# Kernel optimization log

Measured on AMD Instinct MI355X. Metric: run time of the kernel, lower is better.

Reference implementation:

```python
import jax, jax.numpy as jnp
import numpy as np
import math

B, WIN, C_IN, C_OUT = 8, 512, 38, 38
D_MODEL, N_HEADS, E_LAYERS, D_FF = 512, 8, 3, 512
EH = D_MODEL // N_HEADS
LN_EPS = 1e-3  # keras LayerNormalization default


def setup_inputs() -> dict:
    key = jax.random.key(0)
    ks = jax.random.split(key, 24)
    s = 0.02
    rn = lambda k, sh: jax.random.normal(k, sh, jnp.float32) * s
    L, d, H = E_LAYERS, D_MODEL, N_HEADS
    return {
        "x": jax.random.normal(ks[0], (B, WIN, C_IN), jnp.float32),
        "conv_k": rn(ks[1], (3, C_IN, d)),
        "Wq": rn(ks[2], (L, d, d)), "bq": jnp.zeros((L, d), jnp.float32),
        "Wk": rn(ks[3], (L, d, d)), "bk": jnp.zeros((L, d), jnp.float32),
        "Wv": rn(ks[4], (L, d, d)), "bv": jnp.zeros((L, d), jnp.float32),
        "Ws": rn(ks[5], (L, d, H)), "bs": jnp.zeros((L, H), jnp.float32),
        "Wo": rn(ks[6], (L, d, d)), "bo": jnp.zeros((L, d), jnp.float32),
        "W1": rn(ks[7], (L, d, D_FF)), "b1": jnp.zeros((L, D_FF), jnp.float32),
        "W2": rn(ks[8], (L, D_FF, d)), "b2": jnp.zeros((L, d), jnp.float32),
        "ln1_g": jnp.ones((L, d), jnp.float32), "ln1_b": jnp.zeros((L, d), jnp.float32),
        "ln2_g": jnp.ones((L, d), jnp.float32), "ln2_b": jnp.zeros((L, d), jnp.float32),
        "lnf_g": jnp.ones((d,), jnp.float32), "lnf_b": jnp.zeros((d,), jnp.float32),
        "Wp": rn(ks[9], (d, C_OUT)), "bp": jnp.zeros((C_OUT,), jnp.float32),
    }


def _layernorm(x, g, b):
    mu = jnp.mean(x, axis=-1, keepdims=True)
    var = jnp.mean((x - mu) ** 2, axis=-1, keepdims=True)
    return (x - mu) * jax.lax.rsqrt(var + LN_EPS) * g + b


def _pos_embedding():
    pos = jnp.arange(WIN, dtype=jnp.float32)[:, None]
    div = jnp.exp(jnp.arange(0, D_MODEL, 2, dtype=jnp.float32) * (-math.log(10000.0) / D_MODEL))
    # interleave sin at even idx, cos at odd idx
    return jnp.stack([jnp.sin(pos * div), jnp.cos(pos * div)], axis=-1).reshape(WIN, D_MODEL)


def reference(x, conv_k, Wq, bq, Wk, bk, Wv, bv, Ws, bs, Wo, bo,
              W1, b1, W2, b2, ln1_g, ln1_b, ln2_g, ln2_b, lnf_g, lnf_b, Wp, bp):
    # --- DataEmbedding: wrap-pad then Conv1D(k=3, valid), plus sinusoidal PE ---
    xp = jnp.concatenate([x[:, -1:], x, x[:, :1]], axis=1)
    h = jax.lax.conv_general_dilated(xp, conv_k, window_strides=(1,), padding='VALID',
                                     dimension_numbers=('NWC', 'WIO', 'NWC'))
    h = h + _pos_embedding()[None]

    idx = jnp.arange(WIN, dtype=jnp.float32)
    dist = jnp.abs(idx[:, None] - idx[None, :])
    scale = 1.0 / math.sqrt(EH)
    inv_sqrt_2pi = 1.0 / math.sqrt(2.0 * math.pi)

    series_l, prior_l, sigma_l = [], [], []
    for i in range(E_LAYERS):
        q = (h @ Wq[i] + bq[i]).reshape(B, WIN, N_HEADS, EH)
        k = (h @ Wk[i] + bk[i]).reshape(B, WIN, N_HEADS, EH)
        v = (h @ Wv[i] + bv[i]).reshape(B, WIN, N_HEADS, EH)
        sig = h @ Ws[i] + bs[i]

        scores = jnp.einsum('blhe,bshe->bhls', q, k)  # mask_flag=False in model
        series = jax.nn.softmax(scores * scale, axis=-1)  # [B, H, L, S]

        sg = jnp.transpose(sig, (0, 2, 1))               # [B, H, L]
        sg = jax.nn.sigmoid(sg * 5.0) + 1e-5
        sg = jnp.power(3.0, sg) - 1.0
        sg4 = jnp.broadcast_to(sg[..., None], (B, N_HEADS, WIN, WIN))
        prior = inv_sqrt_2pi / sg4 * jnp.exp(-(dist ** 2) / (2.0 * sg4 ** 2))

        attn_out = jnp.einsum('bhls,bshd->blhd', series, v).reshape(B, WIN, D_MODEL)
        h = _layernorm(h + attn_out @ Wo[i] + bo[i], ln1_g[i], ln1_b[i])
        y = jax.nn.gelu(h @ W1[i] + b1[i], approximate=False)
        y = y @ W2[i] + b2[i]
        h = _layernorm(h + y, ln2_g[i], ln2_b[i])

        series_l.append(series); prior_l.append(prior); sigma_l.append(sg4)

    h = _layernorm(h, lnf_g, lnf_b)
    out = h @ Wp + bp
    return (out, jnp.stack(series_l), jnp.stack(prior_l), jnp.stack(sigma_l))
```

## Files before the change

### kernel.cpp

```cpp
#include <hip/hip_runtime.h>
#include <math.h>


typedef unsigned short ushort;
typedef __attribute__((ext_vector_type(8))) ushort ushort8;
typedef __attribute__((ext_vector_type(4))) ushort ushort4v;
typedef __attribute__((ext_vector_type(8))) short short8;
typedef __attribute__((ext_vector_type(4))) float float4v;

__device__ inline ushort f2bf(float f) {
  union { float f; unsigned u; } v; v.f = f;
  return (ushort)((v.u + 0x7fffu + ((v.u >> 16) & 1u)) >> 16);
}

__device__ inline void gload16(const void* g, void* l) {
  __builtin_amdgcn_global_load_lds(
      (const __attribute__((address_space(1))) unsigned int*)g,
      (__attribute__((address_space(3))) unsigned int*)l, 16, 0, 0);
}

__global__ __launch_bounds__(512) void embed_kernel(const float* __restrict__ x,
                                                    const float* __restrict__ ck,
                                                    float* __restrict__ h,
                                                    ushort* __restrict__ hb) {
  int bt = blockIdx.x;
  int b = bt >> 9, t = bt & 511;
  int co = threadIdx.x;
  __shared__ float xs[3][38];
  if (co < 114) {
    int w = co / 38, ci = co - w * 38;
    int r = (t - 1 + w + 512) & 511;
    xs[w][ci] = x[((long)(b << 9) + r) * 38 + ci];
  }
  __syncthreads();
  float acc = 0.f;
#pragma unroll
  for (int w = 0; w < 3; ++w)
#pragma unroll
    for (int ci = 0; ci < 38; ++ci)
      acc = fmaf(xs[w][ci], ck[(w * 38 + ci) * 512 + co], acc);
  float div = expf((float)(co & ~1) * (-9.210340371976184f / 512.f));
  float ang = (float)t * div;
  float pe = (co & 1) ? cosf(ang) : sinf(ang);
  float o = acc + pe;
  h[(long)bt * 512 + co] = o;
  hb[(long)bt * 512 + co] = f2bf(o);
}

__global__ __launch_bounds__(256) void wcvt_kernel(const float* __restrict__ W,
                                                   ushort* __restrict__ Wt,
                                                   long lstride) {
  int l = blockIdx.z;
  int n = blockIdx.x * 256 + threadIdx.x;
  int k0 = blockIdx.y * 8;
  const float* w = W + (long)l * 262144;
  ushort* o = Wt + (long)l * lstride;
  ushort8 v;
#pragma unroll
  for (int i = 0; i < 8; ++i) v[i] = f2bf(w[(long)(k0 + i) * 512 + n]);
  *(ushort8*)&o[(long)n * 512 + k0] = v;
}

__global__ __launch_bounds__(512) void bcat_kernel(const float* __restrict__ bq,
                                                   const float* __restrict__ bk,
                                                   const float* __restrict__ bv,
                                                   float* __restrict__ bqkv) {
  int l = blockIdx.x, t = threadIdx.x;
  bqkv[l * 1536 + t] = bq[l * 512 + t];
  bqkv[l * 1536 + 512 + t] = bk[l * 512 + t];
  bqkv[l * 1536 + 1024 + t] = bv[l * 512 + t];
}

__global__ __launch_bounds__(512) void wst_kernel(const float* __restrict__ Ws,
                                                  float* __restrict__ WsT) {
  int l = blockIdx.x, k = threadIdx.x;
#pragma unroll
  for (int hh = 0; hh < 8; ++hh)
    WsT[(long)l * 4096 + hh * 512 + k] = Ws[(long)l * 4096 + k * 8 + hh];
}

template <bool GELU_, bool CBF16, bool VST>
__global__ __launch_bounds__(256) void gemm_bt(
    const ushort* __restrict__ A, int lda,
    const ushort* __restrict__ B, int ldb,
    const float* __restrict__ bias,
    void* __restrict__ Cv, int ldc, int K,
    ushort* __restrict__ vTout) {
  __shared__ ushort As[2][4096];
  __shared__ ushort Bs[2][2048];
  int t = threadIdx.x;
  int m0 = blockIdx.y * 128, n0 = blockIdx.x * 64;
  int w = t >> 6, lane = t & 63;
  int wr = (w >> 1) * 64, wc = (w & 1) * 32;
  int fm = lane & 15, q4 = lane >> 4;
  float4v acc[4][2];
#pragma unroll
  for (int i = 0; i < 4; ++i)
#pragma unroll
    for (int j = 0; j < 2; ++j) acc[i][j] = (float4v){0.f, 0.f, 0.f, 0.f};

  int kk = (lane & 3) * 8;
  const ushort* ga0 = &A[(long)(m0 + w * 32 + (lane >> 2)) * lda + kk];
  const ushort* ga1 = ga0 + (long)16 * lda;
  const ushort* gb = &B[(long)(n0 + w * 16 + (lane >> 2)) * ldb + kk];

  auto stage = [&](int bi) {
    gload16(ga0, &As[bi][w * 1024]);
    gload16(ga1, &As[bi][w * 1024 + 512]);
    gload16(gb, &Bs[bi][w * 512]);
    ga0 += 32; ga1 += 32; gb += 32;
  };
  auto compute = [&](int bi) {
    short8 a[4], bfr[2];
#pragma unroll
    for (int i = 0; i < 4; ++i)
      a[i] = *(const short8*)&As[bi][(wr + 16 * i + fm) * 32 + q4 * 8];
#pragma unroll
    for (int j = 0; j < 2; ++j)
      bfr[j] = *(const short8*)&Bs[bi][(wc + 16 * j + fm) * 32 + q4 * 8];
#pragma unroll
    for (int i = 0; i < 4; ++i)
#pragma unroll
      for (int j = 0; j < 2; ++j)
        acc[i][j] = __builtin_amdgcn_mfma_f32_16x16x32_bf16(a[i], bfr[j], acc[i][j], 0, 0, 0);
  };

  stage(0);
  __syncthreads();
#pragma unroll 1
  for (int k0 = 0; k0 < K; k0 += 64) {
    stage(1);
    compute(0);
    __syncthreads();
    if (k0 + 64 < K) stage(0);
    compute(1);
    __syncthreads();
  }

#pragma unroll
  for (int j = 0; j < 2; ++j) {
    int col = n0 + wc + 16 * j + fm;
    float bv = bias ? bias[col] : 0.f;
#pragma unroll
    for (int i = 0; i < 4; ++i) {
      int row0 = m0 + wr + 16 * i + q4 * 4;
      float vv[4];
#pragma unroll
      for (int r = 0; r < 4; ++r) {
        float v = acc[i][j][r] + bv;
        if (GELU_) v = 0.5f * v * (1.f + erff(v * 0.7071067811865476f));
        vv[r] = v;
        if (CBF16)
          ((ushort*)Cv)[(long)(row0 + r) * ldc + col] = f2bf(v);
        else
          ((float*)Cv)[(long)(row0 + r) * ldc + col] = v;
      }
      if (VST && n0 >= 1024) {
        int d = (col - 1024) & 63;
        int hh = (n0 - 1024) >> 6;
        int bb = row0 >> 9, s0 = row0 & 511;
        ushort4v pk;
#pragma unroll
        for (int r = 0; r < 4; ++r) pk[r] = f2bf(vv[r]);
        *(ushort4v*)&vTout[((long)(bb * 8 + hh) * 64 + d) * 512 + s0] = pk;
      }
    }
  }
}

__global__ __launch_bounds__(256, 2) void attn_fused(
    const ushort* __restrict__ qkv, const ushort* __restrict__ vT,
    const float* __restrict__ h, const float* __restrict__ WsT,
    const float* __restrict__ bsw,
    float* __restrict__ series, float* __restrict__ prior,
    float* __restrict__ sigma, ushort* __restrict__ t1b) {
  __shared__ ushort Ps[32 * 520];
  __shared__ float red[128];
  __shared__ float sgc[96];

  int t = threadIdx.x;
  int m0 = blockIdx.x * 32;
  int bh = blockIdx.y;
  int b = bh >> 3, hh = bh & 7;
  int w = t >> 6, lane = t & 63;
  int fm = lane & 15, q4 = lane >> 4;
  int wc = w * 128;
  long rowg = (long)b * 512;

  {
    int r = t >> 3, p = t & 7;
    const float* hrow = &h[(rowg + m0 + r) * 512 + p * 64];
    const float* wcol = &WsT[hh * 512 + p * 64];
    float s = 0.f;
#pragma unroll
    for (int i = 0; i < 16; ++i) {
      float4 hv = *(const float4*)&hrow[i * 4];
      float4 wv = *(const float4*)&wcol[i * 4];
      s += hv.x * wv.x + hv.y * wv.y + hv.z * wv.z + hv.w * wv.w;
    }
    s += __shfl_xor(s, 1); s += __shfl_xor(s, 2); s += __shfl_xor(s, 4);
    if (p == 0) {
      float xv = s + bsw[hh];
      float sig = 1.f / (1.f + __expf(-5.f * xv)) + 1e-5f;
      float sgv = expm1f(sig * 1.0986122886681098f);
      sgc[r * 3] = sgv;
      sgc[r * 3 + 1] = 0.3989422804014327f / sgv;
      sgc[r * 3 + 2] = 1.f / sgv;
    }
  }

  float4v acc[2][8];
#pragma unroll
  for (int i = 0; i < 2; ++i)
#pragma unroll
    for (int j = 0; j < 8; ++j) acc[i][j] = (float4v){0.f, 0.f, 0.f, 0.f};

  const ushort* qbase = &qkv[(rowg + m0) * 1536 + hh * 64];
  const ushort* kbase = &qkv[rowg * 1536 + 512 + hh * 64];
#pragma unroll
  for (int ks = 0; ks < 2; ++ks) {
    int ko = ks * 32 + q4 * 8;
    short8 a[2], bfr[8];
#pragma unroll
    for (int i = 0; i < 2; ++i)
      a[i] = *(const short8*)&qbase[(long)(16 * i + fm) * 1536 + ko];
#pragma unroll
    for (int j = 0; j < 8; ++j)
      bfr[j] = *(const short8*)&kbase[(long)(wc + 16 * j + fm) * 1536 + ko];
#pragma unroll
    for (int i = 0; i < 2; ++i)
#pragma unroll
      for (int j = 0; j < 8; ++j)
        acc[i][j] = __builtin_amdgcn_mfma_f32_16x16x32_bf16(a[i], bfr[j], acc[i][j], 0, 0, 0);
  }

#pragma unroll
  for (int i = 0; i < 2; ++i)
#pragma unroll
    for (int j = 0; j < 8; ++j)
#pragma unroll
      for (int r = 0; r < 4; ++r) acc[i][j][r] *= 0.125f;

  float mrow[2][4];
#pragma unroll
  for (int i = 0; i < 2; ++i)
#pragma unroll
    for (int r = 0; r < 4; ++r) {
      float m = acc[i][0][r];
#pragma unroll
      for (int j = 1; j < 8; ++j) m = fmaxf(m, acc[i][j][r]);
#pragma unroll
      for (int off = 1; off < 16; off <<= 1) m = fmaxf(m, __shfl_xor(m, off));
      mrow[i][r] = m;
    }
  if (fm == 0) {
#pragma unroll
    for (int i = 0; i < 2; ++i)
#pragma unroll
      for (int r = 0; r < 4; ++r)
        red[(16 * i + q4 * 4 + r) * 4 + w] = mrow[i][r];
  }
  __syncthreads();
#pragma unroll
  for (int i = 0; i < 2; ++i)
#pragma unroll
    for (int r = 0; r < 4; ++r) {
      const float* rp = &red[(16 * i + q4 * 4 + r) * 4];
      mrow[i][r] = fmaxf(fmaxf(rp[0], rp[1]), fmaxf(rp[2], rp[3]));
    }
  float lrow[2][4];
#pragma unroll
  for (int i = 0; i < 2; ++i)
#pragma unroll
    for (int r = 0; r < 4; ++r) {
      float s = 0.f;
#pragma unroll
      for (int j = 0; j < 8; ++j) {
        float e = __expf(acc[i][j][r] - mrow[i][r]);
        acc[i][j][r] = e;
        s += e;
      }
#pragma unroll
      for (int off = 1; off < 16; off <<= 1) s += __shfl_xor(s, off);
      lrow[i][r] = s;
    }
  __syncthreads();
  if (fm == 0) {
#pragma unroll
    for (int i = 0; i < 2; ++i)
#pragma unroll
      for (int r = 0; r < 4; ++r)
        red[(16 * i + q4 * 4 + r) * 4 + w] = lrow[i][r];
  }
  __syncthreads();
#pragma unroll
  for (int i = 0; i < 2; ++i)
#pragma unroll
    for (int r = 0; r < 4; ++r) {
      const float* rp = &red[(16 * i + q4 * 4 + r) * 4];
      lrow[i][r] = 1.f / (rp[0] + rp[1] + rp[2] + rp[3]);
    }

  float* serp = series + ((long)bh << 18);
#pragma unroll
  for (int i = 0; i < 2; ++i)
#pragma unroll
    for (int r = 0; r < 4; ++r) {
      int row = 16 * i + q4 * 4 + r;
      float inv = lrow[i][r];
#pragma unroll
      for (int j = 0; j < 8; ++j) {
        int col = wc + 16 * j + fm;
        float v = acc[i][j][r] * inv;
        serp[(long)(m0 + row) * 512 + col] = v;
        Ps[row * 520 + col] = f2bf(v);
      }
    }
  __syncthreads();

  float4v acc2[2] = {{0.f, 0.f, 0.f, 0.f}, {0.f, 0.f, 0.f, 0.f}};
  int wn = w * 16;
  const ushort* vbase = &vT[((long)bh * 64 + wn + fm) * 512];
#pragma unroll
  for (int c = 0; c < 8; ++c) {
#pragma unroll
    for (int ks = 0; ks < 2; ++ks) {
      int ko = ks * 32 + q4 * 8;
      short8 b2 = *(const short8*)&vbase[c * 64 + ko];
#pragma unroll
      for (int i = 0; i < 2; ++i) {
        short8 a2 = *(const short8*)&Ps[(16 * i + fm) * 520 + c * 64 + ko];
        acc2[i] = __builtin_amdgcn_mfma_f32_16x16x32_bf16(a2, b2, acc2[i], 0, 0, 0);
      }
    }
  }
#pragma unroll
  for (int i = 0; i < 2; ++i)
#pragma unroll
    for (int r = 0; r < 4; ++r)
      t1b[(rowg + m0 + 16 * i + q4 * 4 + r) * 512 + hh * 64 + wn + fm] =
          f2bf(acc2[i][r]);

  float* prip = prior + ((long)bh << 18);
  float* sigp = sigma + ((long)bh << 18);
  for (int it = t; it < 4096; it += 256) {
    int row = it >> 7;
    int c4 = (it & 127) << 2;
    float sgv = sgc[row * 3], inv = sgc[row * 3 + 1], rinv = sgc[row * 3 + 2];
    float ig = (float)(m0 + row);
    float4 pv, sv;
#pragma unroll
    for (int e = 0; e < 4; ++e) {
      float dd = ig - (float)(c4 + e);
      float rr = dd * rinv;
      ((float*)&pv)[e] = inv * __expf(-0.5f * rr * rr);
      ((float*)&sv)[e] = sgv;
    }
    *(float4*)&prip[(long)(m0 + row) * 512 + c4] = pv;
    *(float4*)&sigp[(long)(m0 + row) * 512 + c4] = sv;
  }
}

__global__ __launch_bounds__(256) void ln_kernel(const float* __restrict__ x,
                                                 const float* __restrict__ delta,
                                                 const float* __restrict__ g,
                                                 const float* __restrict__ bb,
                                                 float* __restrict__ out,
                                                 ushort* __restrict__ hb) {
  long row = blockIdx.x;
  int tid = threadIdx.x;
  int c = tid * 2;
  float2 xv = *(const float2*)&x[row * 512 + c];
  if (delta) {
    float2 dv = *(const float2*)&delta[row * 512 + c];
    xv.x += dv.x; xv.y += dv.y;
  }
  float s = xv.x + xv.y;
  float q = xv.x * xv.x + xv.y * xv.y;
#pragma unroll
  for (int off = 1; off < 64; off <<= 1) {
    s += __shfl_xor(s, off);
    q += __shfl_xor(q, off);
  }
  __shared__ float red[8];
  int wid = tid >> 6;
  if ((tid & 63) == 0) { red[wid] = s; red[wid + 4] = q; }
  __syncthreads();
  float S = red[0] + red[1] + red[2] + red[3];
  float Q = red[4] + red[5] + red[6] + red[7];
  float mean = S * (1.f / 512.f);
  float var = Q * (1.f / 512.f) - mean * mean;
  float rstd = rsqrtf(var + 1e-3f);
  float2 o;
  o.x = (xv.x - mean) * rstd * g[c] + bb[c];
  o.y = (xv.y - mean) * rstd * g[c + 1] + bb[c + 1];
  *(float2*)&out[row * 512 + c] = o;
  if (hb) {
    unsigned pk = ((unsigned)f2bf(o.y) << 16) | (unsigned)f2bf(o.x);
    ((unsigned*)hb)[row * 256 + tid] = pk;
  }
}

template <int NOUT>
__global__ __launch_bounds__(256) void gemm_smallN(const float* __restrict__ A,
                                                   const float* __restrict__ W,
                                                   const float* __restrict__ bias,
                                                   float* __restrict__ C) {
  long row = (long)blockIdx.x * 4 + (threadIdx.x >> 6);
  int lane = threadIdx.x & 63;
  float acc[NOUT];
#pragma unroll
  for (int j = 0; j < NOUT; ++j) acc[j] = 0.f;
  for (int k = lane; k < 512; k += 64) {
    float a = A[row * 512 + k];
    const float* wr = W + (long)k * NOUT;
#pragma unroll
    for (int j = 0; j < NOUT; ++j) acc[j] = fmaf(a, wr[j], acc[j]);
  }
#pragma unroll
  for (int j = 0; j < NOUT; ++j)
#pragma unroll
    for (int off = 32; off; off >>= 1) acc[j] += __shfl_xor(acc[j], off);
  if (lane == 0) {
#pragma unroll
    for (int j = 0; j < NOUT; ++j) C[row * NOUT + j] = acc[j] + bias[j];
  }
}

extern "C" void kernel_launch(void* const* d_in, const int* in_sizes, int n_in,
                              void* d_out, int out_size, void* d_ws, size_t ws_size,
                              hipStream_t stream) {
  (void)in_sizes; (void)n_in; (void)out_size; (void)ws_size;
  const float* x    = (const float*)d_in[0];
  const float* ck   = (const float*)d_in[1];
  const float* Wq   = (const float*)d_in[2];
  const float* bq   = (const float*)d_in[3];
  const float* Wk   = (const float*)d_in[4];
  const float* bk   = (const float*)d_in[5];
  const float* Wv   = (const float*)d_in[6];
  const float* bv   = (const float*)d_in[7];
  const float* Wsw  = (const float*)d_in[8];
  const float* bsw  = (const float*)d_in[9];
  const float* Wo   = (const float*)d_in[10];
  const float* bo   = (const float*)d_in[11];
  const float* W1   = (const float*)d_in[12];
  const float* b1   = (const float*)d_in[13];
  const float* W2   = (const float*)d_in[14];
  const float* b2   = (const float*)d_in[15];
  const float* ln1g = (const float*)d_in[16];
  const float* ln1b = (const float*)d_in[17];
  const float* ln2g = (const float*)d_in[18];
  const float* ln2b = (const float*)d_in[19];
  const float* lnfg = (const float*)d_in[20];
  const float* lnfb = (const float*)d_in[21];
  const float* Wp   = (const float*)d_in[22];
  const float* bp   = (const float*)d_in[23];
  float* out = (float*)d_out;

  float* h    = (float*)d_ws;
  float* t1   = h + 2097152;
  float* t2   = t1 + 2097152;
  float* wst  = t2 + 2097152;
  float* bqkv = wst + 32768;
  ushort* qkv  = (ushort*)(bqkv + 4608);
  ushort* wqkv = qkv + 6291456;
  ushort* wo3  = wqkv + 2359296;
  ushort* w13  = wo3 + 786432;
  ushort* w23  = w13 + 786432;
  ushort* t1b = (ushort*)t1;
  ushort* hb  = (ushort*)(t1 + 1048576);
  ushort* vT  = (ushort*)t2;

  float* series0 = out + 155648;
  float* prior0  = out + 50487296;
  float* sigma0  = out + 100818944;

  dim3 gW(2, 64, 3);
  wcvt_kernel<<<gW, 256, 0, stream>>>(Wq, wqkv, 786432);
  wcvt_kernel<<<gW, 256, 0, stream>>>(Wk, wqkv + 262144, 786432);
  wcvt_kernel<<<gW, 256, 0, stream>>>(Wv, wqkv + 524288, 786432);
  wcvt_kernel<<<gW, 256, 0, stream>>>(Wo, wo3, 262144);
  wcvt_kernel<<<gW, 256, 0, stream>>>(W1, w13, 262144);
  wcvt_kernel<<<gW, 256, 0, stream>>>(W2, w23, 262144);
  bcat_kernel<<<3, 512, 0, stream>>>(bq, bk, bv, bqkv);
  wst_kernel<<<3, 512, 0, stream>>>(Wsw, wst);

  embed_kernel<<<4096, 512, 0, stream>>>(x, ck, h, hb);

  dim3 gQKV(24, 32, 1);
  dim3 gFull(8, 32, 1);
  dim3 gAttn(16, 64, 1);

  for (int l = 0; l < 3; ++l) {
    float* ser = series0 + (long)l * 16777216;
    float* pri = prior0  + (long)l * 16777216;
    float* sgm = sigma0  + (long)l * 16777216;

    gemm_bt<false, true, true><<<gQKV, 256, 0, stream>>>(
        hb, 512, wqkv + (long)l * 786432, 512, bqkv + l * 1536, qkv, 1536, 512, vT);
    attn_fused<<<gAttn, 256, 0, stream>>>(qkv, vT, h, wst + (long)l * 4096,
                                          bsw + (long)l * 8, ser, pri, sgm, t1b);
    gemm_bt<false, false, false><<<gFull, 256, 0, stream>>>(
        t1b, 512, wo3 + (long)l * 262144, 512, bo + (long)l * 512, t2, 512, 512, nullptr);
    ln_kernel<<<4096, 256, 0, stream>>>(h, t2, ln1g + l * 512, ln1b + l * 512, h, hb);
    gemm_bt<true, true, false><<<gFull, 256, 0, stream>>>(
        hb, 512, w13 + (long)l * 262144, 512, b1 + (long)l * 512, t1b, 512, 512, nullptr);
    gemm_bt<false, false, false><<<gFull, 256, 0, stream>>>(
        t1b, 512, w23 + (long)l * 262144, 512, b2 + (long)l * 512, t2, 512, 512, nullptr);
    ln_kernel<<<4096, 256, 0, stream>>>(h, t2, ln2g + l * 512, ln2b + l * 512, h, hb);
  }

  ln_kernel<<<4096, 256, 0, stream>>>(h, nullptr, lnfg, lnfb, t1, nullptr);
  gemm_smallN<38><<<1024, 256, 0, stream>>>(t1, Wp, bp, out);
}
```

Before: 1.037 ms.

## Rewrite GEMM to hold full B tile in LDS, fuse prep and final LN-projection

Replaces the double-buffered bf16 GEMM with a kernel that loads the entire 64x512 weight tile into swizzled LDS once and streams A from global memory into 32x32x16 MFMAs with two split-K accumulators. Weight conversion, bias concatenation and Ws transposes are merged into two launches, and the weight layout is XOR-swizzled to avoid LDS bank conflicts. The final LayerNorm is fused into the output projection kernel. This aims to cut launch overhead and per-k-step syncs, at the cost of 64KB LDS per block limiting occupancy and unstaged A loads from global memory.

Result: slower. 1.063 ms (+2.5%).

```diff
diff --git a/kernel.cpp b/kernel.cpp
--- a/kernel.cpp
+++ b/kernel.cpp
@@ -7,6 +7,7 @@
 typedef __attribute__((ext_vector_type(4))) ushort ushort4v;
 typedef __attribute__((ext_vector_type(8))) short short8;
 typedef __attribute__((ext_vector_type(4))) float float4v;
+typedef __attribute__((ext_vector_type(16))) float float16v;
 
 __device__ inline ushort f2bf(float f) {
   union { float f; unsigned u; } v; v.f = f;
@@ -47,123 +48,118 @@
   hb[(long)bt * 512 + co] = f2bf(o);
 }
 
-__global__ __launch_bounds__(256) void wcvt_kernel(const float* __restrict__ W,
-                                                   ushort* __restrict__ Wt,
-                                                   long lstride) {
-  int l = blockIdx.z;
+__global__ __launch_bounds__(256) void prep_kernel(
+    const float* __restrict__ Wq, const float* __restrict__ Wk,
+    const float* __restrict__ Wv, const float* __restrict__ Wo,
+    const float* __restrict__ W1, const float* __restrict__ W2,
+    ushort* __restrict__ wqkv, ushort* __restrict__ wo3,
+    ushort* __restrict__ w13, ushort* __restrict__ w23) {
+  int z = blockIdx.z;
+  int ten = z / 3, l = z - ten * 3;
+  const float* w;
+  ushort* o;
+  switch (ten) {
+    case 0: w = Wq; o = wqkv + (long)l * 786432; break;
+    case 1: w = Wk; o = wqkv + (long)l * 786432 + 262144; break;
+    case 2: w = Wv; o = wqkv + (long)l * 786432 + 524288; break;
+    case 3: w = Wo; o = wo3 + (long)l * 262144; break;
+    case 4: w = W1; o = w13 + (long)l * 262144; break;
+    default: w = W2; o = w23 + (long)l * 262144; break;
+  }
+  w += (long)l * 262144;
   int n = blockIdx.x * 256 + threadIdx.x;
-  int k0 = blockIdx.y * 8;
-  const float* w = W + (long)l * 262144;
-  ushort* o = Wt + (long)l * lstride;
+  int c = blockIdx.y;
   ushort8 v;
 #pragma unroll
-  for (int i = 0; i < 8; ++i) v[i] = f2bf(w[(long)(k0 + i) * 512 + n]);
-  *(ushort8*)&o[(long)n * 512 + k0] = v;
-}
-
-__global__ __launch_bounds__(512) void bcat_kernel(const float* __restrict__ bq,
-                                                   const float* __restrict__ bk,
-                                                   const float* __restrict__ bv,
-                                                   float* __restrict__ bqkv) {
-  int l = blockIdx.x, t = threadIdx.x;
-  bqkv[l * 1536 + t] = bq[l * 512 + t];
-  bqkv[l * 1536 + 512 + t] = bk[l * 512 + t];
-  bqkv[l * 1536 + 1024 + t] = bv[l * 512 + t];
-}
-
-__global__ __launch_bounds__(512) void wst_kernel(const float* __restrict__ Ws,
-                                                  float* __restrict__ WsT) {
-  int l = blockIdx.x, k = threadIdx.x;
-#pragma unroll
-  for (int hh = 0; hh < 8; ++hh)
-    WsT[(long)l * 4096 + hh * 512 + k] = Ws[(long)l * 4096 + k * 8 + hh];
+  for (int i = 0; i < 8; ++i) v[i] = f2bf(w[(long)(c * 8 + i) * 512 + n]);
+  *(ushort8*)&o[(long)n * 512 + ((c ^ (n & 7)) << 3)] = v;
+}
+
+__global__ __launch_bounds__(512) void bw_kernel(const float* __restrict__ bq,
+                                                 const float* __restrict__ bk,
+                                                 const float* __restrict__ bv,
+                                                 const float* __restrict__ Ws,
+                                                 float* __restrict__ bqkv,
+                                                 float* __restrict__ WsT) {
+  int z = blockIdx.x, t = threadIdx.x;
+  if (z < 3) {
+    bqkv[z * 1536 + t] = bq[z * 512 + t];
+    bqkv[z * 1536 + 512 + t] = bk[z * 512 + t];
+    bqkv[z * 1536 + 1024 + t] = bv[z * 512 + t];
+  } else {
+    int l = z - 3;
+#pragma unroll
+    for (int hh = 0; hh < 8; ++hh)
+      WsT[(long)l * 4096 + hh * 512 + t] = Ws[(long)l * 4096 + t * 8 + hh];
+  }
 }
 
 template <bool GELU_, bool CBF16, bool VST>
-__global__ __launch_bounds__(256) void gemm_bt(
-    const ushort* __restrict__ A, int lda,
-    const ushort* __restrict__ B, int ldb,
+__global__ __launch_bounds__(512, 4) void gemm_wp(
+    const ushort* __restrict__ A,
+    const ushort* __restrict__ B,
     const float* __restrict__ bias,
-    void* __restrict__ Cv, int ldc, int K,
+    void* __restrict__ Cv, int ldc,
     ushort* __restrict__ vTout) {
-  __shared__ ushort As[2][4096];
-  __shared__ ushort Bs[2][2048];
+  __shared__ ushort Bs[32768];
   int t = threadIdx.x;
   int m0 = blockIdx.y * 128, n0 = blockIdx.x * 64;
   int w = t >> 6, lane = t & 63;
-  int wr = (w >> 1) * 64, wc = (w & 1) * 32;
-  int fm = lane & 15, q4 = lane >> 4;
-  float4v acc[4][2];
-#pragma unroll
-  for (int i = 0; i < 4; ++i)
-#pragma unroll
-    for (int j = 0; j < 2; ++j) acc[i][j] = (float4v){0.f, 0.f, 0.f, 0.f};
-
-  int kk = (lane & 3) * 8;
-  const ushort* ga0 = &A[(long)(m0 + w * 32 + (lane >> 2)) * lda + kk];
-  const ushort* ga1 = ga0 + (long)16 * lda;
-  const ushort* gb = &B[(long)(n0 + w * 16 + (lane >> 2)) * ldb + kk];
-
-  auto stage = [&](int bi) {
-    gload16(ga0, &As[bi][w * 1024]);
-    gload16(ga1, &As[bi][w * 1024 + 512]);
-    gload16(gb, &Bs[bi][w * 512]);
-    ga0 += 32; ga1 += 32; gb += 32;
-  };
-  auto compute = [&](int bi) {
-    short8 a[4], bfr[2];
-#pragma unroll
-    for (int i = 0; i < 4; ++i)
-      a[i] = *(const short8*)&As[bi][(wr + 16 * i + fm) * 32 + q4 * 8];
-#pragma unroll
-    for (int j = 0; j < 2; ++j)
-      bfr[j] = *(const short8*)&Bs[bi][(wc + 16 * j + fm) * 32 + q4 * 8];
-#pragma unroll
-    for (int i = 0; i < 4; ++i)
-#pragma unroll
-      for (int j = 0; j < 2; ++j)
-        acc[i][j] = __builtin_amdgcn_mfma_f32_16x16x32_bf16(a[i], bfr[j], acc[i][j], 0, 0, 0);
-  };
-
-  stage(0);
-  __syncthreads();
-#pragma unroll 1
-  for (int k0 = 0; k0 < K; k0 += 64) {
-    stage(1);
-    compute(0);
-    __syncthreads();
-    if (k0 + 64 < K) stage(0);
-    compute(1);
-    __syncthreads();
-  }
-
-#pragma unroll
-  for (int j = 0; j < 2; ++j) {
-    int col = n0 + wc + 16 * j + fm;
-    float bv = bias ? bias[col] : 0.f;
-#pragma unroll
-    for (int i = 0; i < 4; ++i) {
-      int row0 = m0 + wr + 16 * i + q4 * 4;
-      float vv[4];
-#pragma unroll
-      for (int r = 0; r < 4; ++r) {
-        float v = acc[i][j][r] + bv;
-        if (GELU_) v = 0.5f * v * (1.f + erff(v * 0.7071067811865476f));
-        vv[r] = v;
-        if (CBF16)
-          ((ushort*)Cv)[(long)(row0 + r) * ldc + col] = f2bf(v);
-        else
-          ((float*)Cv)[(long)(row0 + r) * ldc + col] = v;
-      }
-      if (VST && n0 >= 1024) {
-        int d = (col - 1024) & 63;
-        int hh = (n0 - 1024) >> 6;
-        int bb = row0 >> 9, s0 = row0 & 511;
-        ushort4v pk;
-#pragma unroll
-        for (int r = 0; r < 4; ++r) pk[r] = f2bf(vv[r]);
-        *(ushort4v*)&vTout[((long)(bb * 8 + hh) * 64 + d) * 512 + s0] = pk;
-      }
+  int l31 = lane & 31, q1 = lane >> 5;
+  int wrow = (w >> 1) * 32, wcol = (w & 1) * 32;
+
+  {
+    const ushort* gb = B + (long)n0 * 512;
+#pragma unroll
+    for (int it = 0; it < 8; ++it)
+      gload16(gb + it * 4096 + t * 8, &Bs[it * 4096 + t * 8]);
+  }
+  __syncthreads();
+
+  float16v acc0, acc1;
+#pragma unroll
+  for (int i = 0; i < 16; ++i) { acc0[i] = 0.f; acc1[i] = 0.f; }
+
+  const ushort* ga = &A[(long)(m0 + wrow + l31) * 512 + q1 * 8];
+  int brow = wcol + l31;
+  int bx = brow & 7;
+  const ushort* bp_ = &Bs[brow * 512];
+
+#pragma unroll
+  for (int k0 = 0; k0 < 512; k0 += 32) {
+    short8 a0 = *(const short8*)&ga[k0];
+    short8 a1 = *(const short8*)&ga[k0 + 16];
+    int kc = (k0 >> 3) + q1;
+    short8 b0 = *(const short8*)&bp_[(kc ^ bx) << 3];
+    short8 b1 = *(const short8*)&bp_[((kc + 2) ^ bx) << 3];
+    acc0 = __builtin_amdgcn_mfma_f32_32x32x16_bf16(a0, b0, acc0, 0, 0, 0);
+    acc1 = __builtin_amdgcn_mfma_f32_32x32x16_bf16(a1, b1, acc1, 0, 0, 0);
+  }
+
+  int col = n0 + wcol + l31;
+  float bvv = bias ? bias[col] : 0.f;
+#pragma unroll
+  for (int rg = 0; rg < 4; ++rg) {
+    int rbase = m0 + wrow + rg * 8 + q1 * 4;
+    float vv[4];
+#pragma unroll
+    for (int rr = 0; rr < 4; ++rr) {
+      float v = acc0[rg * 4 + rr] + acc1[rg * 4 + rr] + bvv;
+      if (GELU_) v = 0.5f * v * (1.f + erff(v * 0.7071067811865476f));
+      vv[rr] = v;
+      if (CBF16)
+        ((ushort*)Cv)[(long)(rbase + rr) * ldc + col] = f2bf(v);
+      else
+        ((float*)Cv)[(long)(rbase + rr) * ldc + col] = v;
+    }
+    if (VST && n0 >= 1024) {
+      int d = wcol + l31;
+      int hh = (n0 - 1024) >> 6;
+      int bb2 = rbase >> 9, s0 = rbase & 511;
+      ushort4v pk;
+#pragma unroll
+      for (int rr = 0; rr < 4; ++rr) pk[rr] = f2bf(vv[rr]);
+      *(ushort4v*)&vTout[((long)(bb2 * 8 + hh) * 64 + d) * 512 + s0] = pk;
     }
   }
 }
@@ -401,29 +397,50 @@
   }
 }
 
-template <int NOUT>
-__global__ __launch_bounds__(256) void gemm_smallN(const float* __restrict__ A,
-                                                   const float* __restrict__ W,
-                                                   const float* __restrict__ bias,
-                                                   float* __restrict__ C) {
+__global__ __launch_bounds__(256) void proj_ln(const float* __restrict__ A,
+                                               const float* __restrict__ g,
+                                               const float* __restrict__ bb,
+                                               const float* __restrict__ W,
+                                               const float* __restrict__ bp,
+                                               float* __restrict__ C) {
   long row = (long)blockIdx.x * 4 + (threadIdx.x >> 6);
   int lane = threadIdx.x & 63;
-  float acc[NOUT];
-#pragma unroll
-  for (int j = 0; j < NOUT; ++j) acc[j] = 0.f;
-  for (int k = lane; k < 512; k += 64) {
-    float a = A[row * 512 + k];
-    const float* wr = W + (long)k * NOUT;
-#pragma unroll
-    for (int j = 0; j < NOUT; ++j) acc[j] = fmaf(a, wr[j], acc[j]);
-  }
-#pragma unroll
-  for (int j = 0; j < NOUT; ++j)
+  int k0 = lane * 8;
+  float xv[8];
+  {
+    float4 x0 = *(const float4*)&A[row * 512 + k0];
+    float4 x1 = *(const float4*)&A[row * 512 + k0 + 4];
+    xv[0] = x0.x; xv[1] = x0.y; xv[2] = x0.z; xv[3] = x0.w;
+    xv[4] = x1.x; xv[5] = x1.y; xv[6] = x1.z; xv[7] = x1.w;
+  }
+  float s = 0.f, q = 0.f;
+#pragma unroll
+  for (int e = 0; e < 8; ++e) { s += xv[e]; q += xv[e] * xv[e]; }
+#pragma unroll
+  for (int off = 1; off < 64; off <<= 1) {
+    s += __shfl_xor(s, off);
+    q += __shfl_xor(q, off);
+  }
+  float mean = s * (1.f / 512.f);
+  float var = q * (1.f / 512.f) - mean * mean;
+  float rstd = rsqrtf(var + 1e-3f);
+  float acc[38];
+#pragma unroll
+  for (int j = 0; j < 38; ++j) acc[j] = 0.f;
+#pragma unroll
+  for (int e = 0; e < 8; ++e) {
+    float xn = (xv[e] - mean) * rstd * g[k0 + e] + bb[k0 + e];
+    const float* wr = &W[(long)(k0 + e) * 38];
+#pragma unroll
+    for (int j = 0; j < 38; ++j) acc[j] = fmaf(xn, wr[j], acc[j]);
+  }
+#pragma unroll
+  for (int j = 0; j < 38; ++j)
 #pragma unroll
     for (int off = 32; off; off >>= 1) acc[j] += __shfl_xor(acc[j], off);
   if (lane == 0) {
 #pragma unroll
-    for (int j = 0; j < NOUT; ++j) C[row * NOUT + j] = acc[j] + bias[j];
+    for (int j = 0; j < 38; ++j) C[row * 38 + j] = acc[j] + bp[j];
   }
 }
 
@@ -475,15 +492,10 @@
   float* prior0  = out + 50487296;
   float* sigma0  = out + 100818944;
 
-  dim3 gW(2, 64, 3);
-  wcvt_kernel<<<gW, 256, 0, stream>>>(Wq, wqkv, 786432);
-  wcvt_kernel<<<gW, 256, 0, stream>>>(Wk, wqkv + 262144, 786432);
-  wcvt_kernel<<<gW, 256, 0, stream>>>(Wv, wqkv + 524288, 786432);
-  wcvt_kernel<<<gW, 256, 0, stream>>>(Wo, wo3, 262144);
-  wcvt_kernel<<<gW, 256, 0, stream>>>(W1, w13, 262144);
-  wcvt_kernel<<<gW, 256, 0, stream>>>(W2, w23, 262144);
-  bcat_kernel<<<3, 512, 0, stream>>>(bq, bk, bv, bqkv);
-  wst_kernel<<<3, 512, 0, stream>>>(Wsw, wst);
+  dim3 gPrep(2, 64, 18);
+  prep_kernel<<<gPrep, 256, 0, stream>>>(Wq, Wk, Wv, Wo, W1, W2,
+                                         wqkv, wo3, w13, w23);
+  bw_kernel<<<6, 512, 0, stream>>>(bq, bk, bv, Wsw, bqkv, wst);
 
   embed_kernel<<<4096, 512, 0, stream>>>(x, ck, h, hb);
 
@@ -496,20 +508,19 @@
     float* pri = prior0  + (long)l * 16777216;
     float* sgm = sigma0  + (long)l * 16777216;
 
-    gemm_bt<false, true, true><<<gQKV, 256, 0, stream>>>(
-        hb, 512, wqkv + (long)l * 786432, 512, bqkv + l * 1536, qkv, 1536, 512, vT);
+    gemm_wp<false, true, true><<<gQKV, 512, 0, stream>>>(
+        hb, wqkv + (long)l * 786432, bqkv + l * 1536, qkv, 1536, vT);
     attn_fused<<<gAttn, 256, 0, stream>>>(qkv, vT, h, wst + (long)l * 4096,
                                           bsw + (long)l * 8, ser, pri, sgm, t1b);
-    gemm_bt<false, false, false><<<gFull, 256, 0, stream>>>(
-        t1b, 512, wo3 + (long)l * 262144, 512, bo + (long)l * 512, t2, 512, 512, nullptr);
+    gemm_wp<false, false, false><<<gFull, 512, 0, stream>>>(
+        t1b, wo3 + (long)l * 262144, bo + (long)l * 512, t2, 512, nullptr);
     ln_kernel<<<4096, 256, 0, stream>>>(h, t2, ln1g + l * 512, ln1b + l * 512, h, hb);
-    gemm_bt<true, true, false><<<gFull, 256, 0, stream>>>(
-        hb, 512, w13 + (long)l * 262144, 512, b1 + (long)l * 512, t1b, 512, 512, nullptr);
-    gemm_bt<false, false, false><<<gFull, 256, 0, stream>>>(
-        t1b, 512, w23 + (long)l * 262144, 512, b2 + (long)l * 512, t2, 512, 512, nullptr);
+    gemm_wp<true, true, false><<<gFull, 512, 0, stream>>>(
+        hb, w13 + (long)l * 262144, b1 + (long)l * 512, t1b, 512, nullptr);
+    gemm_wp<false, false, false><<<gFull, 512, 0, stream>>>(
+        t1b, w23 + (long)l * 262144, b2 + (long)l * 512, t2, 512, nullptr);
     ln_kernel<<<4096, 256, 0, stream>>>(h, t2, ln2g + l * 512, ln2b + l * 512, h, hb);
   }
 
-  ln_kernel<<<4096, 256, 0, stream>>>(h, nullptr, lnfg, lnfb, t1, nullptr);
-  gemm_smallN<38><<<1024, 256, 0, stream>>>(t1, Wp, bp, out);
-}
+  proj_ln<<<1024, 256, 0, stream>>>(h, lnfg, lnfb, Wp, bp, out);
+}
```

## Merge prep kernels, fuse final LN into projection, use nontemporal output stores

Applied to the files above, without the earlier changes.

The six weight-conversion launches become one launch, and the bias-concat and Ws-transpose kernels are merged into another, which cuts launch overhead. The final layernorm is fused into the 38-output projection kernel, so the normalized activations are no longer written out and read back. The large series/prior/sigma output writes in the attention kernel now use nontemporal stores to reduce cache pollution from streaming writes. The fused projection keeps 38 accumulators per thread, which raises register pressure.

Result: faster. 1.012 ms (-2.4%).

```diff
diff --git a/kernel.cpp b/kernel.cpp
--- a/kernel.cpp
+++ b/kernel.cpp
@@ -47,36 +47,50 @@
   hb[(long)bt * 512 + co] = f2bf(o);
 }
 
-__global__ __launch_bounds__(256) void wcvt_kernel(const float* __restrict__ W,
-                                                   ushort* __restrict__ Wt,
-                                                   long lstride) {
-  int l = blockIdx.z;
+__global__ __launch_bounds__(256) void prep_kernel(
+    const float* __restrict__ Wq, const float* __restrict__ Wk,
+    const float* __restrict__ Wv, const float* __restrict__ Wo,
+    const float* __restrict__ W1, const float* __restrict__ W2,
+    ushort* __restrict__ wqkv, ushort* __restrict__ wo3,
+    ushort* __restrict__ w13, ushort* __restrict__ w23) {
+  int z = blockIdx.z;
+  int ten = z / 3, l = z - ten * 3;
+  const float* w;
+  ushort* o;
+  switch (ten) {
+    case 0: w = Wq; o = wqkv + (long)l * 786432; break;
+    case 1: w = Wk; o = wqkv + (long)l * 786432 + 262144; break;
+    case 2: w = Wv; o = wqkv + (long)l * 786432 + 524288; break;
+    case 3: w = Wo; o = wo3 + (long)l * 262144; break;
+    case 4: w = W1; o = w13 + (long)l * 262144; break;
+    default: w = W2; o = w23 + (long)l * 262144; break;
+  }
+  w += (long)l * 262144;
   int n = blockIdx.x * 256 + threadIdx.x;
-  int k0 = blockIdx.y * 8;
-  const float* w = W + (long)l * 262144;
-  ushort* o = Wt + (long)l * lstride;
+  int c = blockIdx.y;
   ushort8 v;
 #pragma unroll
-  for (int i = 0; i < 8; ++i) v[i] = f2bf(w[(long)(k0 + i) * 512 + n]);
-  *(ushort8*)&o[(long)n * 512 + k0] = v;
-}
-
-__global__ __launch_bounds__(512) void bcat_kernel(const float* __restrict__ bq,
-                                                   const float* __restrict__ bk,
-                                                   const float* __restrict__ bv,
-                                                   float* __restrict__ bqkv) {
-  int l = blockIdx.x, t = threadIdx.x;
-  bqkv[l * 1536 + t] = bq[l * 512 + t];
-  bqkv[l * 1536 + 512 + t] = bk[l * 512 + t];
-  bqkv[l * 1536 + 1024 + t] = bv[l * 512 + t];
-}
-
-__global__ __launch_bounds__(512) void wst_kernel(const float* __restrict__ Ws,
-                                                  float* __restrict__ WsT) {
-  int l = blockIdx.x, k = threadIdx.x;
-#pragma unroll
-  for (int hh = 0; hh < 8; ++hh)
-    WsT[(long)l * 4096 + hh * 512 + k] = Ws[(long)l * 4096 + k * 8 + hh];
+  for (int i = 0; i < 8; ++i) v[i] = f2bf(w[(long)(c * 8 + i) * 512 + n]);
+  *(ushort8*)&o[(long)n * 512 + c * 8] = v;
+}
+
+__global__ __launch_bounds__(512) void bw_kernel(const float* __restrict__ bq,
+                                                 const float* __restrict__ bk,
+                                                 const float* __restrict__ bv,
+                                                 const float* __restrict__ Ws,
+                                                 float* __restrict__ bqkv,
+                                                 float* __restrict__ WsT) {
+  int z = blockIdx.x, t = threadIdx.x;
+  if (z < 3) {
+    bqkv[z * 1536 + t] = bq[z * 512 + t];
+    bqkv[z * 1536 + 512 + t] = bk[z * 512 + t];
+    bqkv[z * 1536 + 1024 + t] = bv[z * 512 + t];
+  } else {
+    int l = z - 3;
+#pragma unroll
+    for (int hh = 0; hh < 8; ++hh)
+      WsT[(long)l * 4096 + hh * 512 + t] = Ws[(long)l * 4096 + t * 8 + hh];
+  }
 }
 
 template <bool GELU_, bool CBF16, bool VST>
@@ -312,7 +326,7 @@
       for (int j = 0; j < 8; ++j) {
         int col = wc + 16 * j + fm;
         float v = acc[i][j][r] * inv;
-        serp[(long)(m0 + row) * 512 + col] = v;
+        __builtin_nontemporal_store(v, &serp[(long)(m0 + row) * 512 + col]);
         Ps[row * 520 + col] = f2bf(v);
       }
     }
@@ -348,16 +362,16 @@
     int c4 = (it & 127) << 2;
     float sgv = sgc[row * 3], inv = sgc[row * 3 + 1], rinv = sgc[row * 3 + 2];
     float ig = (float)(m0 + row);
-    float4 pv, sv;
+    float4v pv, sv;
 #pragma unroll
     for (int e = 0; e < 4; ++e) {
       float dd = ig - (float)(c4 + e);
       float rr = dd * rinv;
-      ((float*)&pv)[e] = inv * __expf(-0.5f * rr * rr);
-      ((float*)&sv)[e] = sgv;
-    }
-    *(float4*)&prip[(long)(m0 + row) * 512 + c4] = pv;
-    *(float4*)&sigp[(long)(m0 + row) * 512 + c4] = sv;
+      pv[e] = inv * __expf(-0.5f * rr * rr);
+      sv[e] = sgv;
+    }
+    __builtin_nontemporal_store(pv, (float4v*)&prip[(long)(m0 + row) * 512 + c4]);
+    __builtin_nontemporal_store(sv, (float4v*)&sigp[(long)(m0 + row) * 512 + c4]);
   }
 }
 
@@ -401,29 +415,50 @@
   }
 }
 
-template <int NOUT>
-__global__ __launch_bounds__(256) void gemm_smallN(const float* __restrict__ A,
-                                                   const float* __restrict__ W,
-                                                   const float* __restrict__ bias,
-                                                   float* __restrict__ C) {
+__global__ __launch_bounds__(256) void proj_ln(const float* __restrict__ A,
+                                               const float* __restrict__ g,
+                                               const float* __restrict__ bb,
+                                               const float* __restrict__ W,
+                                               const float* __restrict__ bp,
+                                               float* __restrict__ C) {
   long row = (long)blockIdx.x * 4 + (threadIdx.x >> 6);
   int lane = threadIdx.x & 63;
-  float acc[NOUT];
-#pragma unroll
-  for (int j = 0; j < NOUT; ++j) acc[j] = 0.f;
-  for (int k = lane; k < 512; k += 64) {
-    float a = A[row * 512 + k];
-    const float* wr = W + (long)k * NOUT;
-#pragma unroll
-    for (int j = 0; j < NOUT; ++j) acc[j] = fmaf(a, wr[j], acc[j]);
-  }
-#pragma unroll
-  for (int j = 0; j < NOUT; ++j)
+  int k0 = lane * 8;
+  float xv[8];
+  {
+    float4 x0 = *(const float4*)&A[row * 512 + k0];
+    float4 x1 = *(const float4*)&A[row * 512 + k0 + 4];
+    xv[0] = x0.x; xv[1] = x0.y; xv[2] = x0.z; xv[3] = x0.w;
+    xv[4] = x1.x; xv[5] = x1.y; xv[6] = x1.z; xv[7] = x1.w;
+  }
+  float s = 0.f, q = 0.f;
+#pragma unroll
+  for (int e = 0; e < 8; ++e) { s += xv[e]; q += xv[e] * xv[e]; }
+#pragma unroll
+  for (int off = 1; off < 64; off <<= 1) {
+    s += __shfl_xor(s, off);
+    q += __shfl_xor(q, off);
+  }
+  float mean = s * (1.f / 512.f);
+  float var = q * (1.f / 512.f) - mean * mean;
+  float rstd = rsqrtf(var + 1e-3f);
+  float acc[38];
+#pragma unroll
+  for (int j = 0; j < 38; ++j) acc[j] = 0.f;
+#pragma unroll
+  for (int e = 0; e < 8; ++e) {
+    float xn = (xv[e] - mean) * rstd * g[k0 + e] + bb[k0 + e];
+    const float* wr = &W[(long)(k0 + e) * 38];
+#pragma unroll
+    for (int j = 0; j < 38; ++j) acc[j] = fmaf(xn, wr[j], acc[j]);
+  }
+#pragma unroll
+  for (int j = 0; j < 38; ++j)
 #pragma unroll
     for (int off = 32; off; off >>= 1) acc[j] += __shfl_xor(acc[j], off);
   if (lane == 0) {
 #pragma unroll
-    for (int j = 0; j < NOUT; ++j) C[row * NOUT + j] = acc[j] + bias[j];
+    for (int j = 0; j < 38; ++j) C[row * 38 + j] = acc[j] + bp[j];
   }
 }
 
@@ -475,15 +510,10 @@
   float* prior0  = out + 50487296;
   float* sigma0  = out + 100818944;
 
-  dim3 gW(2, 64, 3);
-  wcvt_kernel<<<gW, 256, 0, stream>>>(Wq, wqkv, 786432);
-  wcvt_kernel<<<gW, 256, 0, stream>>>(Wk, wqkv + 262144, 786432);
-  wcvt_kernel<<<gW, 256, 0, stream>>>(Wv, wqkv + 524288, 786432);
-  wcvt_kernel<<<gW, 256, 0, stream>>>(Wo, wo3, 262144);
-  wcvt_kernel<<<gW, 256, 0, stream>>>(W1, w13, 262144);
-  wcvt_kernel<<<gW, 256, 0, stream>>>(W2, w23, 262144);
-  bcat_kernel<<<3, 512, 0, stream>>>(bq, bk, bv, bqkv);
-  wst_kernel<<<3, 512, 0, stream>>>(Wsw, wst);
+  dim3 gPrep(2, 64, 18);
+  prep_kernel<<<gPrep, 256, 0, stream>>>(Wq, Wk, Wv, Wo, W1, W2,
+                                         wqkv, wo3, w13, w23);
+  bw_kernel<<<6, 512, 0, stream>>>(bq, bk, bv, Wsw, bqkv, wst);
 
   embed_kernel<<<4096, 512, 0, stream>>>(x, ck, h, hb);
 
@@ -510,6 +540,5 @@
     ln_kernel<<<4096, 256, 0, stream>>>(h, t2, ln2g + l * 512, ln2b + l * 512, h, hb);
   }
 
-  ln_kernel<<<4096, 256, 0, stream>>>(h, nullptr, lnfg, lnfb, t1, nullptr);
-  gemm_smallN<38><<<1024, 256, 0, stream>>>(t1, Wp, bp, out);
-}
+  proj_ln<<<1024, 256, 0, stream>>>(h, lnfg, lnfb, Wp, bp, out);
+}
```
